# Kernel tuning notes

Hardware: AMD Instinct MI355X
Metric: run time of the kernel (lower is better)

## Reference

```python
import jax, jax.numpy as jnp
import numpy as np

D_HEAD = 64
EPS_NORM = 1e-6
EPS_COS = 1e-6


def rms_norm(x, scale, eps=EPS_NORM):
    mean_sq = jnp.mean(x * x, axis=-1, keepdims=True)
    return x * (scale * jax.lax.rsqrt(mean_sq + eps))


def setup_inputs() -> dict:
    key = jax.random.key(0)
    ks = jax.random.split(key, 8)
    b, l, d, d_ff = 2, 2048, 1024, 3072
    std = 1.0 / np.sqrt(d)
    return {
        "x": jax.random.normal(ks[0], (b, l, d), jnp.float32),
        "pos": jax.random.normal(ks[1], (b, l, 2), jnp.float32),
        "norm_scale": jnp.ones((d,), jnp.float32),
        "w_qkv": jax.random.normal(ks[2], (3 * d, d), jnp.float32) * std,
        "attn_scale": jnp.full((d // D_HEAD,), 10.0, jnp.float32),
        "w_out": jax.random.normal(ks[3], (d, d), jnp.float32) * std,
        "ff_norm_scale": jnp.ones((d,), jnp.float32),
        "w_up": jax.random.normal(ks[4], (2 * d_ff, d), jnp.float32) * std,
        "w_down": jax.random.normal(ks[5], (d, d_ff), jnp.float32) * (1.0 / np.sqrt(d_ff)),
    }


def reference(x, pos, norm_scale, w_qkv, attn_scale, w_out, ff_norm_scale, w_up, w_down):
    n, l, d = x.shape
    nh = d // D_HEAD

    # ---- self-attention block ----
    skip = x
    xn = rms_norm(x, norm_scale)
    qkv = xn @ w_qkv.T                                    # [n, l, 3d]
    qkv = qkv.reshape(n, l, 3, nh, D_HEAD).transpose(2, 0, 3, 1, 4)  # [3, n, nh, l, e]
    q, k, v = qkv[0], qkv[1], qkv[2]

    # cosine-similarity rescaling with per-head learned scale
    s = attn_scale[:, None, None]                         # [nh, 1, 1]
    sqrt_s = jnp.sqrt(s)
    q = q * (sqrt_s * jax.lax.rsqrt(jnp.sum(q * q, axis=-1, keepdims=True) + EPS_COS))
    k = k * (sqrt_s * jax.lax.rsqrt(jnp.sum(k * k, axis=-1, keepdims=True) + EPS_COS))

    # SDPA with scale=1.0 (no RoPE: rope_cls=None)
    scores = jnp.einsum("nhqe,nhke->nhqk", q, k)
    attn = jax.nn.softmax(scores, axis=-1)
    o = jnp.einsum("nhqk,nhke->nhqe", attn, v)            # [n, nh, l, e]
    o = o.transpose(0, 2, 1, 3).reshape(n, l, d)
    x = o @ w_out.T + skip

    # ---- feed-forward block (SwiGLU) ----
    skip = x
    xn = rms_norm(x, ff_norm_scale)
    u = xn @ w_up.T                                       # [n, l, 2*d_ff]
    a, g = jnp.split(u, 2, axis=-1)
    h = a * jax.nn.silu(g)
    x = h @ w_down.T + skip
    return x
```

## Files before the change

kernel.cpp:

```cpp
#include <hip/hip_runtime.h>
#include <cstdint>
#include <cstddef>
#include <cstdio>


typedef unsigned short u16;
typedef __bf16 bf16x8 __attribute__((ext_vector_type(8)));
typedef short  s16x4  __attribute__((ext_vector_type(4)));
typedef float  f32x4  __attribute__((ext_vector_type(4)));

__device__ __forceinline__ u16 f2b(float f) {
  return __builtin_bit_cast(u16, (__bf16)f);
}
__device__ __forceinline__ float b2f(u16 u) {
  return (float)__builtin_bit_cast(__bf16, u);
}

__device__ __forceinline__ void cp16(const u16* g, u16* l) {
  __builtin_amdgcn_global_load_lds(
      (__attribute__((address_space(1))) void*)(uintptr_t)g,
      (__attribute__((address_space(3))) void*)(uintptr_t)l,
      16, 0, 0);
}

template <int MODE, int BN>
__global__ __launch_bounds__(256) void gemm_bt(
    const u16* __restrict__ A, const u16* __restrict__ B,
    float* __restrict__ Cf, u16* __restrict__ Cb, const float* __restrict__ res,
    int M, int N, int K, int lda)
{
  constexpr int NI = BN / 32;
  __shared__ __align__(16) u16 lsA[128 * 64];
  __shared__ __align__(16) u16 lsB[BN * 64];
  const int t = threadIdx.x;
  const int w = t >> 6, lane = t & 63;
  const int wm = (w >> 1) * 64, wn = (w & 1) * (BN / 2);
  const int lr = lane & 15, quad = lane >> 4;
  const int cswz = lr & 7;
  const size_t rowA0 = (size_t)blockIdx.x * 128;
  const size_t rowB0 = (size_t)blockIdx.y * BN;

  f32x4 acc[4][NI] = {};

  for (int k0 = 0; k0 < K; k0 += 64) {
#pragma unroll
    for (int i = 0; i < 4; ++i) {
      const int id = i * 256 + t;
      const int r = id >> 3;
      const int c = ((id & 7) ^ (r & 7)) * 8;
      cp16(A + (rowA0 + r) * lda + k0 + c, lsA + id * 8);
    }
#pragma unroll
    for (int i = 0; i < BN / 32; ++i) {
      const int id = i * 256 + t;
      const int r = id >> 3;
      const int c = ((id & 7) ^ (r & 7)) * 8;
      cp16(B + (rowB0 + r) * (size_t)K + k0 + c, lsB + id * 8);
    }
    __syncthreads();
#pragma unroll
    for (int ks = 0; ks < 2; ++ks) {
      const int co = ((ks * 4 + quad) ^ cswz) * 8;
      bf16x8 af[4], bfr[NI];
#pragma unroll
      for (int i = 0; i < 4; ++i)
        af[i] = *(const bf16x8*)(lsA + (wm + i * 16 + lr) * 64 + co);
#pragma unroll
      for (int i = 0; i < NI; ++i)
        bfr[i] = *(const bf16x8*)(lsB + (wn + i * 16 + lr) * 64 + co);
#pragma unroll
      for (int mi = 0; mi < 4; ++mi)
#pragma unroll
        for (int ni = 0; ni < NI; ++ni)
          acc[mi][ni] = __builtin_amdgcn_mfma_f32_16x16x32_bf16(
              af[mi], bfr[ni], acc[mi][ni], 0, 0, 0);
    }
    __syncthreads();
  }

#pragma unroll
  for (int mi = 0; mi < 4; ++mi) {
#pragma unroll
    for (int r = 0; r < 4; ++r) {
      const size_t m = rowA0 + wm + mi * 16 + quad * 4 + r;
#pragma unroll
      for (int ni = 0; ni < NI; ++ni) {
        const size_t n = rowB0 + wn + ni * 16 + lr;
        const size_t o = m * (size_t)N + n;
        const float v = acc[mi][ni][r];
        if (MODE == 0) Cf[o] = v;
        else if (MODE == 1) Cf[o] = v + res[o];
        else Cb[o] = f2b(v);
      }
    }
  }
}

__global__ __launch_bounds__(256) void rmsnorm_k(
    const float* __restrict__ x, const float* __restrict__ g, u16* __restrict__ out)
{
  const int row = blockIdx.x;
  const int t = threadIdx.x;
  const float4 a = ((const float4*)(x + (size_t)row * 1024))[t];
  float ss = a.x * a.x + a.y * a.y + a.z * a.z + a.w * a.w;
#pragma unroll
  for (int o = 32; o; o >>= 1) ss += __shfl_xor(ss, o, 64);
  __shared__ float red[4];
  if ((t & 63) == 0) red[t >> 6] = ss;
  __syncthreads();
  ss = red[0] + red[1] + red[2] + red[3];
  const float r = rsqrtf(ss * (1.0f / 1024.0f) + 1e-6f);
  const float4 gg = ((const float4*)g)[t];
  ushort4 o4;
  o4.x = f2b(a.x * gg.x * r);
  o4.y = f2b(a.y * gg.y * r);
  o4.z = f2b(a.z * gg.z * r);
  o4.w = f2b(a.w * gg.w * r);
  ((ushort4*)out)[(size_t)row * 256 + t] = o4;
}

__global__ __launch_bounds__(256) void cvt_bf16_k(
    const float* __restrict__ in, u16* __restrict__ out)
{
  const size_t i = (size_t)blockIdx.x * 256 + threadIdx.x;
  const float4 v = ((const float4*)in)[i];
  ushort4 o4;
  o4.x = f2b(v.x); o4.y = f2b(v.y); o4.z = f2b(v.z); o4.w = f2b(v.w);
  ((ushort4*)out)[i] = o4;
}

__global__ __launch_bounds__(256) void qkv_prep_k(
    const u16* __restrict__ qkv, const float* __restrict__ attn_scale,
    u16* __restrict__ Qb, u16* __restrict__ Kb, u16* __restrict__ Vt)
{
  const int l0 = blockIdx.x * 64;
  const int h  = blockIdx.y;
  const int nb = blockIdx.z;
  const int t = threadIdx.x, w = t >> 6, lane = t & 63;
  __shared__ float lsV[64][65];
  const float sq = sqrtf(attn_scale[h]);
  const int head = nb * 16 + h;
#pragma unroll 4
  for (int i = 0; i < 16; ++i) {
    const int lrow = i * 4 + w;
    const int l = l0 + lrow;
    const u16* base = qkv + ((size_t)nb * 2048 + l) * 3072 + h * 64 + lane;
    const float qv = b2f(base[0]);
    const float kv = b2f(base[1024]);
    const float vv = b2f(base[2048]);
    float ssq = qv * qv, ssk = kv * kv;
#pragma unroll
    for (int o = 32; o; o >>= 1) {
      ssq += __shfl_xor(ssq, o, 64);
      ssk += __shfl_xor(ssk, o, 64);
    }
    const size_t gb = ((size_t)head * 2048 + l) * 64 + lane;
    Qb[gb] = f2b(qv * sq * rsqrtf(ssq + 1e-6f));
    Kb[gb] = f2b(kv * sq * rsqrtf(ssk + 1e-6f));
    lsV[lrow][lane] = vv;
  }
  __syncthreads();
  const int e = t >> 2, p = t & 3;
  union { u16 s[16]; uint4 v[2]; } tmp;
#pragma unroll
  for (int j = 0; j < 16; ++j) tmp.s[j] = f2b(lsV[p * 16 + j][e]);
  u16* dst = Vt + ((size_t)head * 64 + e) * 2048 + l0 + p * 16;
  *(uint4*)dst = tmp.v[0];
  *(uint4*)(dst + 8) = tmp.v[1];
}

__global__ __launch_bounds__(256) void attn_k(
    const u16* __restrict__ Qb, const u16* __restrict__ Kb,
    const u16* __restrict__ Vt, u16* __restrict__ O)
{
  const int l0 = blockIdx.x * 64;
  const int head = blockIdx.y;
  const int nb = head >> 4, h = head & 15;
  const int t = threadIdx.x, w = t >> 6, lane = t & 63;
  const int lr = lane & 15, quad = lane >> 4;
  __shared__ __align__(16) u16 lsK[2][64 * 64];
  __shared__ __align__(16) u16 lsV[2][64 * 64];
  const size_t hb = (size_t)head << 17;

  const int sr = t >> 3;
  const int sc = ((t & 7) ^ (sr & 7)) * 8;
  const u16* Kg = Kb + hb + (size_t)sr * 64 + sc;
  const u16* Vg = Vt + hb + (size_t)sr * 2048 + sc;

  const int qrow = l0 + w * 16 + lr;
  const u16* qp = Qb + hb + (size_t)qrow * 64 + quad * 8;
  const bf16x8 qf0 = *(const bf16x8*)qp;
  const bf16x8 qf1 = *(const bf16x8*)(qp + 32);

  f32x4 ot[4] = {};
  float rs = 0.f;

  cp16(Kg, lsK[0] + t * 8);
  cp16(Kg + 32 * 64, lsK[0] + 32 * 64 + t * 8);
  cp16(Vg, lsV[0] + t * 8);
  cp16(Vg + 32 * 2048, lsV[0] + 32 * 64 + t * 8);

  int cur = 0;
  for (int k0 = 0; k0 < 2048; k0 += 64) {
    __syncthreads();
    if (k0 + 64 < 2048) {
      const int nxt = cur ^ 1;
      const u16* Kn = Kg + (size_t)(k0 + 64) * 64;
      const u16* Vn = Vg + (k0 + 64);
      cp16(Kn, lsK[nxt] + t * 8);
      cp16(Kn + 32 * 64, lsK[nxt] + 32 * 64 + t * 8);
      cp16(Vn, lsV[nxt] + t * 8);
      cp16(Vn + 32 * 2048, lsV[nxt] + 32 * 64 + t * 8);
    }
    const u16* kb = lsK[cur];
    const u16* vb = lsV[cur];

#pragma unroll
    for (int kt = 0; kt < 4; ++kt) {
      const int krow = (kt * 16 + lr) * 64;
      const int kswz = lr & 7;
      const bf16x8 a0 = *(const bf16x8*)(kb + krow + ((quad ^ kswz) << 3));
      const bf16x8 a1 = *(const bf16x8*)(kb + krow + (((4 + quad) ^ kswz) << 3));
      f32x4 s = {};
      s = __builtin_amdgcn_mfma_f32_16x16x32_bf16(a0, qf0, s, 0, 0, 0);
      s = __builtin_amdgcn_mfma_f32_16x16x32_bf16(a1, qf1, s, 0, 0, 0);
      s16x4 pf;
#pragma unroll
      for (int r = 0; r < 4; ++r) {
        const float p = __expf(s[r]);
        rs += p;
        pf[r] = (short)f2b(p);
      }
      const int vc = kt * 2 + (quad >> 1);
      const int vh = (quad & 1) * 4;
#pragma unroll
      for (int ei = 0; ei < 4; ++ei) {
        const int vrow = ei * 16 + lr;
        const s16x4 vf = *(const s16x4*)(vb + vrow * 64 + ((vc ^ (vrow & 7)) << 3) + vh);
        ot[ei] = __builtin_amdgcn_mfma_f32_16x16x16bf16_1k(vf, pf, ot[ei], 0, 0, 0);
      }
    }
    cur ^= 1;
  }

  rs += __shfl_xor(rs, 16, 64);
  rs += __shfl_xor(rs, 32, 64);
  const float inv = 1.0f / rs;

  u16* ob = O + ((size_t)nb * 2048 + l0 + w * 16 + lr) * 1024 + h * 64 + quad * 4;
#pragma unroll
  for (int ei = 0; ei < 4; ++ei) {
    ushort4 o4;
    o4.x = f2b(ot[ei][0] * inv);
    o4.y = f2b(ot[ei][1] * inv);
    o4.z = f2b(ot[ei][2] * inv);
    o4.w = f2b(ot[ei][3] * inv);
    *(ushort4*)(ob + ei * 16) = o4;
  }
}

__global__ __launch_bounds__(256) void swiglu_k(u16* __restrict__ u)
{
  const unsigned j = ((unsigned)blockIdx.x * 256 + threadIdx.x) * 8;
  const unsigned row = j / 3072u, col = j % 3072u;
  u16* ap = u + (size_t)row * 6144 + col;
  union { u16 s[8]; uint4 v; } a, g, hh;
  a.v = *(const uint4*)ap;
  g.v = *(const uint4*)(ap + 3072);
#pragma unroll
  for (int i = 0; i < 8; ++i) {
    const float av = b2f(a.s[i]);
    const float gv = b2f(g.s[i]);
    hh.s[i] = f2b(av * (gv / (1.0f + __expf(-gv))));
  }
  *(uint4*)ap = hh.v;
}

static constexpr size_t WQKV_B = 0;
static constexpr size_t WOUT_B = WQKV_B + 6291456;
static constexpr size_t WUP_B  = WOUT_B + 2097152;
static constexpr size_t WDN_B  = WUP_B + 12582912;
static constexpr size_t XN_B   = WDN_B + 6291456;
static constexpr size_t Q_B    = XN_B + 8388608;
static constexpr size_t K_B    = Q_B + 8388608;
static constexpr size_t VT_B   = K_B + 8388608;
static constexpr size_t O_B    = VT_B + 8388608;
static constexpr size_t BIG_B  = O_B + 8388608;
static constexpr size_t WS_NEED = BIG_B + 50331648;

extern "C" void kernel_launch(void* const* d_in, const int* in_sizes, int n_in,
                              void* d_out, int out_size, void* d_ws, size_t ws_size,
                              hipStream_t stream)
{
  (void)in_sizes; (void)n_in; (void)out_size;
  if (ws_size < WS_NEED) {
    fprintf(stderr, "kernel_launch: ws_size %zu < required %zu\n", ws_size, WS_NEED);
    return;
  }
  const float* x          = (const float*)d_in[0];
  const float* norm_scale = (const float*)d_in[2];
  const float* w_qkv      = (const float*)d_in[3];
  const float* attn_scale = (const float*)d_in[4];
  const float* w_out      = (const float*)d_in[5];
  const float* ff_scale   = (const float*)d_in[6];
  const float* w_up       = (const float*)d_in[7];
  const float* w_down     = (const float*)d_in[8];
  float* out = (float*)d_out;
  char* ws = (char*)d_ws;

  u16* wqkv_b = (u16*)(ws + WQKV_B);
  u16* wout_b = (u16*)(ws + WOUT_B);
  u16* wup_b  = (u16*)(ws + WUP_B);
  u16* wdn_b  = (u16*)(ws + WDN_B);
  u16* xn     = (u16*)(ws + XN_B);
  u16* Qb     = (u16*)(ws + Q_B);
  u16* Kb     = (u16*)(ws + K_B);
  u16* Vtb    = (u16*)(ws + VT_B);
  u16* Ob     = (u16*)(ws + O_B);
  u16* qkvb   = (u16*)(ws + BIG_B);
  u16* ub     = (u16*)(ws + BIG_B);

  cvt_bf16_k<<<3072, 256, 0, stream>>>(w_qkv, wqkv_b);
  cvt_bf16_k<<<1024, 256, 0, stream>>>(w_out, wout_b);
  cvt_bf16_k<<<6144, 256, 0, stream>>>(w_up,  wup_b);
  cvt_bf16_k<<<3072, 256, 0, stream>>>(w_down, wdn_b);

  rmsnorm_k<<<4096, 256, 0, stream>>>(x, norm_scale, xn);
  gemm_bt<2, 128><<<dim3(32, 24), 256, 0, stream>>>(xn, wqkv_b, nullptr, qkvb,
                                                    nullptr, 4096, 3072, 1024, 1024);
  qkv_prep_k<<<dim3(32, 16, 2), 256, 0, stream>>>(qkvb, attn_scale, Qb, Kb, Vtb);
  attn_k<<<dim3(32, 32), 256, 0, stream>>>(Qb, Kb, Vtb, Ob);
  gemm_bt<1, 64><<<dim3(32, 16), 256, 0, stream>>>(Ob, wout_b, out, nullptr, x,
                                                   4096, 1024, 1024, 1024);
  rmsnorm_k<<<4096, 256, 0, stream>>>(out, ff_scale, xn);
  gemm_bt<2, 128><<<dim3(32, 48), 256, 0, stream>>>(xn, wup_b, nullptr, ub, nullptr,
                                                    4096, 6144, 1024, 1024);
  swiglu_k<<<6144, 256, 0, stream>>>(ub);
  gemm_bt<1, 64><<<dim3(32, 16), 256, 0, stream>>>(ub, wdn_b, out, nullptr, out,
                                                   4096, 1024, 3072, 6144);
}
```

Measured before the change: 368.5 us.

## Split attention KV tile across warps, permute V layout, split-K down-projection with atomics

The attention kernel now has each warp cover 32 query rows and half of each 64-key tile. This lets each K/V fragment loaded from LDS feed two query blocks, with the two key halves merged through shared memory at the end. The V transpose in the prep kernel is permuted so that each PV step can read V with one 8-wide load instead of two 4-wide ones. The down-projection GEMM switches to split-K (two K slices) with BN=128 and atomicAdd into the output, which already holds the residual. This trades atomic traffic and non-deterministic summation order for better reuse and occupancy.

Result: slower. 378.7 us (+2.8%).

```diff
diff --git a/kernel.cpp b/kernel.cpp
--- a/kernel.cpp
+++ b/kernel.cpp
@@ -7,6 +7,7 @@
 typedef unsigned short u16;
 typedef __bf16 bf16x8 __attribute__((ext_vector_type(8)));
 typedef short  s16x4  __attribute__((ext_vector_type(4)));
+typedef short  s16x8  __attribute__((ext_vector_type(8)));
 typedef float  f32x4  __attribute__((ext_vector_type(4)));
 
 __device__ __forceinline__ u16 f2b(float f) {
@@ -39,10 +40,12 @@
   const int cswz = lr & 7;
   const size_t rowA0 = (size_t)blockIdx.x * 128;
   const size_t rowB0 = (size_t)blockIdx.y * BN;
+  const int kpb = K / (int)gridDim.z;
+  const int kz0 = (int)blockIdx.z * kpb;
 
   f32x4 acc[4][NI] = {};
 
-  for (int k0 = 0; k0 < K; k0 += 64) {
+  for (int k0 = kz0; k0 < kz0 + kpb; k0 += 64) {
 #pragma unroll
     for (int i = 0; i < 4; ++i) {
       const int id = i * 256 + t;
@@ -90,7 +93,8 @@
         const float v = acc[mi][ni][r];
         if (MODE == 0) Cf[o] = v;
         else if (MODE == 1) Cf[o] = v + res[o];
-        else Cb[o] = f2b(v);
+        else if (MODE == 2) Cb[o] = f2b(v);
+        else atomicAdd(&Cf[o], v);
       }
     }
   }
@@ -163,7 +167,15 @@
   const int e = t >> 2, p = t & 3;
   union { u16 s[16]; uint4 v[2]; } tmp;
 #pragma unroll
-  for (int j = 0; j < 16; ++j) tmp.s[j] = f2b(lsV[p * 16 + j][e]);
+  for (int cc = 0; cc < 2; ++cc) {
+    const int c = 2 * p + cc;
+    const int kb = 32 * (c >> 2) + 4 * (c & 3);
+#pragma unroll
+    for (int i = 0; i < 4; ++i) {
+      tmp.s[cc * 8 + i]     = f2b(lsV[kb + i][e]);
+      tmp.s[cc * 8 + 4 + i] = f2b(lsV[kb + 16 + i][e]);
+    }
+  }
   u16* dst = Vt + ((size_t)head * 64 + e) * 2048 + l0 + p * 16;
   *(uint4*)dst = tmp.v[0];
   *(uint4*)(dst + 8) = tmp.v[1];
@@ -178,8 +190,8 @@
   const int nb = head >> 4, h = head & 15;
   const int t = threadIdx.x, w = t >> 6, lane = t & 63;
   const int lr = lane & 15, quad = lane >> 4;
-  __shared__ __align__(16) u16 lsK[2][64 * 64];
-  __shared__ __align__(16) u16 lsV[2][64 * 64];
+  const int kh = w & 1, qh = w >> 1;
+  __shared__ __align__(16) u16 lsKV[2][2][64 * 64];
   const size_t hb = (size_t)head << 17;
 
   const int sr = t >> 3;
@@ -187,18 +199,21 @@
   const u16* Kg = Kb + hb + (size_t)sr * 64 + sc;
   const u16* Vg = Vt + hb + (size_t)sr * 2048 + sc;
 
-  const int qrow = l0 + w * 16 + lr;
-  const u16* qp = Qb + hb + (size_t)qrow * 64 + quad * 8;
-  const bf16x8 qf0 = *(const bf16x8*)qp;
-  const bf16x8 qf1 = *(const bf16x8*)(qp + 32);
-
-  f32x4 ot[4] = {};
-  float rs = 0.f;
-
-  cp16(Kg, lsK[0] + t * 8);
-  cp16(Kg + 32 * 64, lsK[0] + 32 * 64 + t * 8);
-  cp16(Vg, lsV[0] + t * 8);
-  cp16(Vg + 32 * 2048, lsV[0] + 32 * 64 + t * 8);
+  bf16x8 qf[2][2];
+#pragma unroll
+  for (int qb = 0; qb < 2; ++qb) {
+    const u16* qp = Qb + hb + (size_t)(l0 + qh * 32 + qb * 16 + lr) * 64 + quad * 8;
+    qf[qb][0] = *(const bf16x8*)qp;
+    qf[qb][1] = *(const bf16x8*)(qp + 32);
+  }
+
+  f32x4 ot[2][4] = {};
+  float rs[2] = {0.f, 0.f};
+
+  cp16(Kg, lsKV[0][0] + t * 8);
+  cp16(Kg + 32 * 64, lsKV[0][0] + 32 * 64 + t * 8);
+  cp16(Vg, lsKV[0][1] + t * 8);
+  cp16(Vg + 32 * 2048, lsKV[0][1] + 32 * 64 + t * 8);
 
   int cur = 0;
   for (int k0 = 0; k0 < 2048; k0 += 64) {
@@ -207,55 +222,87 @@
       const int nxt = cur ^ 1;
       const u16* Kn = Kg + (size_t)(k0 + 64) * 64;
       const u16* Vn = Vg + (k0 + 64);
-      cp16(Kn, lsK[nxt] + t * 8);
-      cp16(Kn + 32 * 64, lsK[nxt] + 32 * 64 + t * 8);
-      cp16(Vn, lsV[nxt] + t * 8);
-      cp16(Vn + 32 * 2048, lsV[nxt] + 32 * 64 + t * 8);
-    }
-    const u16* kb = lsK[cur];
-    const u16* vb = lsV[cur];
-
-#pragma unroll
-    for (int kt = 0; kt < 4; ++kt) {
+      cp16(Kn, lsKV[nxt][0] + t * 8);
+      cp16(Kn + 32 * 64, lsKV[nxt][0] + 32 * 64 + t * 8);
+      cp16(Vn, lsKV[nxt][1] + t * 8);
+      cp16(Vn + 32 * 2048, lsKV[nxt][1] + 32 * 64 + t * 8);
+    }
+    const u16* kb = lsKV[cur][0];
+    const u16* vb = lsKV[cur][1];
+
+    s16x4 pf[2][2];
+#pragma unroll
+    for (int ktl = 0; ktl < 2; ++ktl) {
+      const int kt = kh * 2 + ktl;
       const int krow = (kt * 16 + lr) * 64;
       const int kswz = lr & 7;
       const bf16x8 a0 = *(const bf16x8*)(kb + krow + ((quad ^ kswz) << 3));
       const bf16x8 a1 = *(const bf16x8*)(kb + krow + (((4 + quad) ^ kswz) << 3));
-      f32x4 s = {};
-      s = __builtin_amdgcn_mfma_f32_16x16x32_bf16(a0, qf0, s, 0, 0, 0);
-      s = __builtin_amdgcn_mfma_f32_16x16x32_bf16(a1, qf1, s, 0, 0, 0);
-      s16x4 pf;
-#pragma unroll
-      for (int r = 0; r < 4; ++r) {
-        const float p = __expf(s[r]);
-        rs += p;
-        pf[r] = (short)f2b(p);
+#pragma unroll
+      for (int qb = 0; qb < 2; ++qb) {
+        f32x4 s = {};
+        s = __builtin_amdgcn_mfma_f32_16x16x32_bf16(a0, qf[qb][0], s, 0, 0, 0);
+        s = __builtin_amdgcn_mfma_f32_16x16x32_bf16(a1, qf[qb][1], s, 0, 0, 0);
+#pragma unroll
+        for (int r = 0; r < 4; ++r) {
+          const float p = __expf(s[r]);
+          rs[qb] += p;
+          pf[qb][ktl][r] = (short)f2b(p);
+        }
       }
-      const int vc = kt * 2 + (quad >> 1);
-      const int vh = (quad & 1) * 4;
+    }
+#pragma unroll
+    for (int ei = 0; ei < 4; ++ei) {
+      const int vrow = ei * 16 + lr;
+      const s16x8 vv = *(const s16x8*)(vb + vrow * 64 + (((kh * 4 + quad) ^ (vrow & 7)) << 3));
+      const s16x4 v0 = __builtin_shufflevector(vv, vv, 0, 1, 2, 3);
+      const s16x4 v1 = __builtin_shufflevector(vv, vv, 4, 5, 6, 7);
+#pragma unroll
+      for (int qb = 0; qb < 2; ++qb) {
+        ot[qb][ei] = __builtin_amdgcn_mfma_f32_16x16x16bf16_1k(v0, pf[qb][0], ot[qb][ei], 0, 0, 0);
+        ot[qb][ei] = __builtin_amdgcn_mfma_f32_16x16x16bf16_1k(v1, pf[qb][1], ot[qb][ei], 0, 0, 0);
+      }
+    }
+    cur ^= 1;
+  }
+
+#pragma unroll
+  for (int qb = 0; qb < 2; ++qb) {
+    rs[qb] += __shfl_xor(rs[qb], 16, 64);
+    rs[qb] += __shfl_xor(rs[qb], 32, 64);
+  }
+
+  __syncthreads();
+  float* mb = (float*)lsKV;
+  if (kh == 1) {
+    float* dst = mb + (qh * 64 + lane) * 34;
+#pragma unroll
+    for (int qb = 0; qb < 2; ++qb)
+#pragma unroll
+      for (int ei = 0; ei < 4; ++ei)
+#pragma unroll
+        for (int r = 0; r < 4; ++r)
+          dst[qb * 16 + ei * 4 + r] = ot[qb][ei][r];
+    dst[32] = rs[0];
+    dst[33] = rs[1];
+  }
+  __syncthreads();
+  if (kh == 0) {
+    const float* src = mb + (qh * 64 + lane) * 34;
+#pragma unroll
+    for (int qb = 0; qb < 2; ++qb) {
+      const float inv = 1.0f / (rs[qb] + src[32 + qb]);
+      u16* ob = O + ((size_t)nb * 2048 + l0 + qh * 32 + qb * 16 + lr) * 1024 + h * 64 + quad * 4;
 #pragma unroll
       for (int ei = 0; ei < 4; ++ei) {
-        const int vrow = ei * 16 + lr;
-        const s16x4 vf = *(const s16x4*)(vb + vrow * 64 + ((vc ^ (vrow & 7)) << 3) + vh);
-        ot[ei] = __builtin_amdgcn_mfma_f32_16x16x16bf16_1k(vf, pf, ot[ei], 0, 0, 0);
+        ushort4 o4;
+        o4.x = f2b((ot[qb][ei][0] + src[qb * 16 + ei * 4 + 0]) * inv);
+        o4.y = f2b((ot[qb][ei][1] + src[qb * 16 + ei * 4 + 1]) * inv);
+        o4.z = f2b((ot[qb][ei][2] + src[qb * 16 + ei * 4 + 2]) * inv);
+        o4.w = f2b((ot[qb][ei][3] + src[qb * 16 + ei * 4 + 3]) * inv);
+        *(ushort4*)(ob + ei * 16) = o4;
       }
     }
-    cur ^= 1;
-  }
-
-  rs += __shfl_xor(rs, 16, 64);
-  rs += __shfl_xor(rs, 32, 64);
-  const float inv = 1.0f / rs;
-
-  u16* ob = O + ((size_t)nb * 2048 + l0 + w * 16 + lr) * 1024 + h * 64 + quad * 4;
-#pragma unroll
-  for (int ei = 0; ei < 4; ++ei) {
-    ushort4 o4;
-    o4.x = f2b(ot[ei][0] * inv);
-    o4.y = f2b(ot[ei][1] * inv);
-    o4.z = f2b(ot[ei][2] * inv);
-    o4.w = f2b(ot[ei][3] * inv);
-    *(ushort4*)(ob + ei * 16) = o4;
   }
 }
 
@@ -336,6 +383,6 @@
   gemm_bt<2, 128><<<dim3(32, 48), 256, 0, stream>>>(xn, wup_b, nullptr, ub, nullptr,
                                                     4096, 6144, 1024, 1024);
   swiglu_k<<<6144, 256, 0, stream>>>(ub);
-  gemm_bt<1, 64><<<dim3(32, 16), 256, 0, stream>>>(ub, wdn_b, out, nullptr, out,
-                                                   4096, 1024, 3072, 6144);
-}
+  gemm_bt<3, 128><<<dim3(32, 8, 2), 256, 0, stream>>>(ub, wdn_b, out, nullptr,
+                                                      nullptr, 4096, 1024, 3072, 6144);
+}
```
